# Performance work log

Measured on AMD Instinct MI355X. Metric: run time of the kernel, lower is better.

## Reference

```python
import math
import jax, jax.numpy as jnp
import numpy as np

N_HEAD = 16
KNN = 4                     # config.knn_num
MEM_FRAC = 8.0              # config.mem_frac
INFLUENCE = 1.0             # config.knn_softmax_influence
RESID_FOUND = 0.5           # from set_resid_frac(resid_frac=0.5) (assumed split)
RESID_CURR = 0.5


def setup_inputs() -> dict:
    key = jax.random.key(0)
    ks = jax.random.split(key, 7)
    B, T, C, H, M = 1, 1024, 1024, N_HEAD, 8192
    d = C // H
    return {
        "x": jax.random.normal(ks[0], (B, T, C), jnp.float32),
        "c_attn_w": jax.random.normal(ks[1], (3 * C, C), jnp.float32) * 0.02,
        "c_attn_b": jax.random.normal(ks[2], (3 * C,), jnp.float32) * 0.01,
        "c_proj_w": jax.random.normal(ks[3], (C, C), jnp.float32) * 0.02,
        "c_proj_b": jax.random.normal(ks[4], (C,), jnp.float32) * 0.01,
        "key_store": jax.random.normal(ks[5], (H, M, d), jnp.float32),
        "value_store": jax.random.normal(ks[6], (H, M, d), jnp.float32),
    }


def _knn_get(att, k, q, v, key_store, value_store):
    # Faithful vectorized version of knn_get (batch must be 1, as in the
    # original whose scatter offsets i*t are only valid for b==1).
    B, H, T, d = k.shape
    scale = 1.0 / math.sqrt(d)
    # last-query attention row over all keys: (B,H,T)
    a = att[:, :, -1, :]
    # mem_frac thresholding (bookkeeping_frac falsy -> skipped)
    a = jnp.where(a < 1.0 / (MEM_FRAC * T), 0.0, a)
    sel = (a != 0.0)[0]                      # (H,T) selected positions
    kh, qh, vh = k[0], q[0], v[0]            # (H,T,d)
    # exact L2 search = faiss.IndexFlatL2: d2 = |k|^2 - 2 k.s + |s|^2
    d2 = (jnp.sum(kh * kh, -1, keepdims=True)
          - 2.0 * jnp.einsum('htd,hmd->htm', kh, key_store)
          + jnp.sum(key_store * key_store, -1)[:, None, :])   # (H,T,M)
    _, idx = jax.lax.top_k(-d2, KNN)         # (H,T,K) nearest neighbors
    idx = jnp.maximum(idx, 0)                # idx[idx<0]=0
    keys_f = jnp.take_along_axis(key_store[:, None, :, :], idx[..., None], axis=2)   # (H,T,K,d)
    vals_f = jnp.take_along_axis(value_store[:, None, :, :], idx[..., None], axis=2)
    # not resid_only: prepend current key/value -> stack size K+1
    keys_all = jnp.concatenate([kh[:, :, None, :], keys_f], axis=2)   # (H,T,S,d)
    vals_all = jnp.concatenate([vh[:, :, None, :], vals_f], axis=2)
    attf = jnp.einsum('htd,htsd->hts', qh, keys_all) * scale
    attf = jnp.where(jnp.isnan(attf), -jnp.inf, attf)
    w = jax.nn.softmax(attf * INFLUENCE, axis=-1)                     # softmax over the stack dim
    vals = jnp.einsum('hts,htsd->htd', w, vals_all)
    vals = vals * RESID_FOUND + vh * RESID_CURR                       # resid mix branch
    v_new = jnp.where(sel[..., None], vals, vh)                       # scatter back
    return v_new[None]                                                # (1,H,T,d)


def reference(x, c_attn_w, c_attn_b, c_proj_w, c_proj_b, key_store, value_store):
    B, T, C = x.shape
    H = key_store.shape[0]
    d = C // H
    qkv = x @ c_attn_w.T + c_attn_b
    q, k, v = jnp.split(qkv, 3, axis=2)
    heads = lambda t: t.reshape(B, T, H, d).transpose(0, 2, 1, 3)
    q, k, v = heads(q), heads(k), heads(v)
    logits = jnp.einsum('bhqd,bhkd->bhqk', q, k) * (1.0 / math.sqrt(d))
    causal = jnp.tril(jnp.ones((T, T), bool))
    logits = jnp.where(causal, logits, -jnp.inf)
    att = jax.nn.softmax(logits, axis=-1)
    # knn_get runs under torch.no_grad in the original
    v_new = jax.lax.stop_gradient(_knn_get(att, k, q, v, key_store, value_store))
    y = jnp.einsum('bhqk,bhkd->bhqd', att, v_new)   # dropout p=0 (eval)
    y = y.transpose(0, 2, 1, 3).reshape(B, T, C)
    return y @ c_proj_w.T + c_proj_b
```

## Files before the change

kernel.cpp:

```cpp
#include <hip/hip_runtime.h>
#include <math.h>

#define NH 16
#define TT 1024
#define CC 1024
#define DD 64
#define MM 8192
#define MQ 4
#define MQS (MM / MQ)

typedef __attribute__((ext_vector_type(8))) short short8;
typedef __attribute__((ext_vector_type(4))) float f32x4;

__device__ __forceinline__ float wredsum(float x) {
#pragma unroll
  for (int o = 32; o; o >>= 1) x += __shfl_xor(x, o);
  return x;
}
__device__ __forceinline__ unsigned int bf16rn(float x) {
  unsigned int u = __float_as_uint(x);
  return (u + 0x7fffu + ((u >> 16) & 1u)) >> 16;
}
__device__ __forceinline__ float bf16f(unsigned int h) {
  return __uint_as_float(h << 16);
}

__device__ __forceinline__ void ins4(float d, int i, float vd[4], int vi[4]) {
  if (d < vd[3] || (d == vd[3] && i < vi[3])) {
    vd[3] = d; vi[3] = i;
#pragma unroll
    for (int s = 3; s > 0; --s) {
      bool sw = (vd[s] < vd[s - 1]) || (vd[s] == vd[s - 1] && vi[s] < vi[s - 1]);
      if (sw) {
        float td = vd[s]; vd[s] = vd[s - 1]; vd[s - 1] = td;
        int ti = vi[s]; vi[s] = vi[s - 1]; vi[s - 1] = ti;
      }
    }
  }
}

__device__ __forceinline__ void stage_rows8_swz(const char* gRow0, size_t gStride, char* lds, int lane) {
  int rr = lane >> 3;
  int c = (lane & 7) ^ rr;
  __builtin_amdgcn_global_load_lds(
      (const __attribute__((address_space(1))) unsigned int*)(gRow0 + (size_t)rr * gStride + (c << 4)),
      (__attribute__((address_space(3))) unsigned int*)lds, 16, 0, 0);
}

__device__ __forceinline__ void conv_chunk(const float* __restrict__ src,
                                           char* __restrict__ hi, char* __restrict__ lo, int gc) {
  const float* p = src + ((size_t)gc << 3);
  float4 f0 = *(const float4*)p;
  float4 f1 = *(const float4*)(p + 4);
  float f[8] = {f0.x, f0.y, f0.z, f0.w, f1.x, f1.y, f1.z, f1.w};
  short8 hv, lv;
#pragma unroll
  for (int e = 0; e < 8; ++e) {
    unsigned hb = bf16rn(f[e]);
    hv[e] = (short)hb;
    lv[e] = (short)bf16rn(f[e] - bf16f(hb));
  }
  size_t off = (size_t)gc << 4;
  *(short8*)(hi + off) = hv;
  *(short8*)(lo + off) = lv;
}

__global__ void __launch_bounds__(256) convert_all(
    const float* __restrict__ x, char* __restrict__ xhi, char* __restrict__ xlo,
    const float* __restrict__ Wa, char* __restrict__ wahi, char* __restrict__ walo,
    const float* __restrict__ Wp, char* __restrict__ wphi, char* __restrict__ wplo)
{
  int b = blockIdx.x, tid = threadIdx.x;
  if (b < 512) conv_chunk(x, xhi, xlo, b * 256 + tid);
  else if (b < 2048) conv_chunk(Wa, wahi, walo, (b - 512) * 256 + tid);
  else conv_chunk(Wp, wphi, wplo, (b - 2048) * 256 + tid);
}

__global__ void __launch_bounds__(256) convert_kernel(
    const float* __restrict__ ks, char* __restrict__ khi,
    char* __restrict__ klo, float* __restrict__ kn2)
{
  int gc = blockIdx.x * 256 + threadIdx.x;
  const float* p = ks + ((size_t)gc << 3);
  float4 f0 = *(const float4*)p;
  float4 f1 = *(const float4*)(p + 4);
  float f[8] = {f0.x, f0.y, f0.z, f0.w, f1.x, f1.y, f1.z, f1.w};
  float s = 0.f;
  short8 hv, lv;
#pragma unroll
  for (int e = 0; e < 8; ++e) {
    s = fmaf(f[e], f[e], s);
    unsigned hb = bf16rn(f[e]);
    hv[e] = (short)hb;
    lv[e] = (short)bf16rn(f[e] - bf16f(hb));
  }
  size_t off = (size_t)gc << 4;
  *(short8*)(khi + off) = hv;
  *(short8*)(klo + off) = lv;
  s += __shfl_xor(s, 1);
  s += __shfl_xor(s, 2);
  s += __shfl_xor(s, 4);
  if ((threadIdx.x & 7) == 0) kn2[gc >> 3] = -0.5f * s;
}

__global__ void __launch_bounds__(256) gemm_hl(
    const char* __restrict__ Ahi, const char* __restrict__ Alo, int strideA, int aKb0, int aKbz,
    const char* __restrict__ Bhi, const char* __restrict__ Blo, int strideB, int bKb0, int bKbz,
    int kbBeg, int kbCnt, int kbzStep,
    float* __restrict__ Cf, long long czMul, int ldc,
    const float* __restrict__ bias, float scale)
{
  int bx = blockIdx.x, by = blockIdx.y, z = blockIdx.z;
  int n0 = bx * 128, m0 = by * 128;
  int tid = threadIdx.x, lane = tid & 63, w = tid >> 6;
  int wr = w >> 1, wc = w & 1;
  __shared__ __align__(16) char smem[65536];
  char* sAhi = smem;
  char* sAlo = smem + 16384;
  char* sBhi = smem + 32768;
  char* sBlo = smem + 49152;
  f32x4 acc[4][4];
#pragma unroll
  for (int i = 0; i < 4; ++i)
#pragma unroll
    for (int j = 0; j < 4; ++j) acc[i][j] = (f32x4){0.f, 0.f, 0.f, 0.f};

  int kb0 = kbBeg + z * kbzStep;
  int lr = lane & 15, lc = lane >> 4;
  for (int i = 0; i < kbCnt; ++i) {
    int kbA = aKb0 + z * aKbz + kb0 + i;
    int kbB = bKb0 + z * bKbz + kb0 + i;
    if (i) __syncthreads();
#pragma unroll
    for (int c8 = 0; c8 < 4; ++c8) {
      int r8 = w * 32 + c8 * 8;
      stage_rows8_swz(Ahi + (size_t)(m0 + r8) * strideA + (size_t)kbA * 128, strideA, sAhi + r8 * 128, lane);
      stage_rows8_swz(Alo + (size_t)(m0 + r8) * strideA + (size_t)kbA * 128, strideA, sAlo + r8 * 128, lane);
      stage_rows8_swz(Bhi + (size_t)(n0 + r8) * strideB + (size_t)kbB * 128, strideB, sBhi + r8 * 128, lane);
      stage_rows8_swz(Blo + (size_t)(n0 + r8) * strideB + (size_t)kbB * 128, strideB, sBlo + r8 * 128, lane);
    }
    __syncthreads();
#pragma unroll
    for (int kh = 0; kh < 2; ++kh) {
      short8 ah[4], al[4], bh[4], bl[4];
#pragma unroll
      for (int f = 0; f < 4; ++f) {
        int ra = wr * 64 + f * 16 + lr;
        int ca = ((kh * 4 + lc) ^ (ra & 7)) << 4;
        ah[f] = *(const short8*)(sAhi + ra * 128 + ca);
        al[f] = *(const short8*)(sAlo + ra * 128 + ca);
        int rb = wc * 64 + f * 16 + lr;
        int cb = ((kh * 4 + lc) ^ (rb & 7)) << 4;
        bh[f] = *(const short8*)(sBhi + rb * 128 + cb);
        bl[f] = *(const short8*)(sBlo + rb * 128 + cb);
      }
#pragma unroll
      for (int mi = 0; mi < 4; ++mi)
#pragma unroll
        for (int nj = 0; nj < 4; ++nj) {
          acc[mi][nj] = __builtin_amdgcn_mfma_f32_16x16x32_bf16(ah[mi], bh[nj], acc[mi][nj], 0, 0, 0);
          acc[mi][nj] = __builtin_amdgcn_mfma_f32_16x16x32_bf16(al[mi], bh[nj], acc[mi][nj], 0, 0, 0);
          acc[mi][nj] = __builtin_amdgcn_mfma_f32_16x16x32_bf16(ah[mi], bl[nj], acc[mi][nj], 0, 0, 0);
        }
    }
  }
#pragma unroll
  for (int mi = 0; mi < 4; ++mi)
#pragma unroll
    for (int nj = 0; nj < 4; ++nj)
#pragma unroll
      for (int r = 0; r < 4; ++r) {
        int m = m0 + wr * 64 + mi * 16 + lc * 4 + r;
        int n = n0 + wc * 64 + nj * 16 + lr;
        float v = acc[mi][nj][r] * scale;
        if (bias) v += bias[n];
        Cf[(size_t)z * czMul + (size_t)m * ldc + n] = v;
      }
}

__global__ void __launch_bounds__(256) reduce_qkv(
    const float* __restrict__ p, const float* __restrict__ bias,
    char* __restrict__ hi, char* __restrict__ lo)
{
  int gc = blockIdx.x * 256 + threadIdx.x;
  int t = gc / 384, c = gc - t * 384;
  const float* p0 = p + (size_t)t * 3072 + (c << 3);
  const float* p1 = p0 + (size_t)3072 * 1024;
  float4 a0 = *(const float4*)p0, a1 = *(const float4*)(p0 + 4);
  float4 b0 = *(const float4*)p1, b1 = *(const float4*)(p1 + 4);
  float4 bb0 = *(const float4*)(bias + (c << 3));
  float4 bb1 = *(const float4*)(bias + (c << 3) + 4);
  float f[8] = {a0.x + b0.x + bb0.x, a0.y + b0.y + bb0.y,
                a0.z + b0.z + bb0.z, a0.w + b0.w + bb0.w,
                a1.x + b1.x + bb1.x, a1.y + b1.y + bb1.y,
                a1.z + b1.z + bb1.z, a1.w + b1.w + bb1.w};
  short8 hv, lv;
#pragma unroll
  for (int e = 0; e < 8; ++e) {
    unsigned hb = bf16rn(f[e]);
    hv[e] = (short)hb;
    lv[e] = (short)bf16rn(f[e] - bf16f(hb));
  }
  size_t off = (size_t)gc << 4;
  *(short8*)(hi + off) = hv;
  *(short8*)(lo + off) = lv;
}

#define QSLDS 2304
__global__ void __launch_bounds__(512) qk_softmax(
    const char* __restrict__ qhi, const char* __restrict__ qlo,
    char* __restrict__ attB, float* __restrict__ attlast)
{
  int rb = blockIdx.x, h = blockIdx.y;
  int i0 = rb * 32;
  int tid = threadIdx.x, lane = tid & 63, w = tid >> 6;
  int wr = w >> 2, wcg = w & 3;
  int lr = lane & 15, lc = lane >> 4;
  __shared__ float redm[2][16][4];
  __shared__ float reds[2][16][4];
  __shared__ __align__(16) char tb[8][2 * QSLDS];

  int iq = i0 + wr * 16 + lr;
  short8 ah[2], al[2];
  {
    size_t qb = (size_t)iq * 6144 + h * 128;
#pragma unroll
    for (int kh = 0; kh < 2; ++kh) {
      size_t off = qb + ((kh * 4 + lc) << 4);
      ah[kh] = *(const short8*)(qhi + off);
      al[kh] = *(const short8*)(qlo + off);
    }
  }

  f32x4 acc[16];
#pragma unroll
  for (int nt = 0; nt < 16; ++nt) acc[nt] = (f32x4){0.f, 0.f, 0.f, 0.f};

  int maxj = i0 + 31;
#pragma unroll
  for (int nt = 0; nt < 16; ++nt) {
    if (wcg * 256 + nt * 16 <= maxj) {
      int jr = wcg * 256 + nt * 16 + lr;
      size_t kb = (size_t)jr * 6144 + 2048 + h * 128;
      short8 bh[2], bl[2];
#pragma unroll
      for (int kh = 0; kh < 2; ++kh) {
        size_t off = kb + ((kh * 4 + lc) << 4);
        bh[kh] = *(const short8*)(qhi + off);
        bl[kh] = *(const short8*)(qlo + off);
      }
#pragma unroll
      for (int kh = 0; kh < 2; ++kh) {
        acc[nt] = __builtin_amdgcn_mfma_f32_16x16x32_bf16(ah[kh], bh[kh], acc[nt], 0, 0, 0);
        acc[nt] = __builtin_amdgcn_mfma_f32_16x16x32_bf16(al[kh], bh[kh], acc[nt], 0, 0, 0);
        acc[nt] = __builtin_amdgcn_mfma_f32_16x16x32_bf16(ah[kh], bl[kh], acc[nt], 0, 0, 0);
      }
    }
  }

  int iv[4];
  float pmax[4];
#pragma unroll
  for (int r = 0; r < 4; ++r) {
    iv[r] = i0 + wr * 16 + lc * 4 + r;
    pmax[r] = -INFINITY;
  }
#pragma unroll
  for (int nt = 0; nt < 16; ++nt) {
    int j = wcg * 256 + nt * 16 + lr;
#pragma unroll
    for (int r = 0; r < 4; ++r) {
      float v = (j <= iv[r]) ? acc[nt][r] * 0.125f : -INFINITY;
      acc[nt][r] = v;
      pmax[r] = fmaxf(pmax[r], v);
    }
  }
#pragma unroll
  for (int o = 1; o <= 8; o <<= 1)
#pragma unroll
    for (int r = 0; r < 4; ++r) pmax[r] = fmaxf(pmax[r], __shfl_xor(pmax[r], o));
  if (lr == 0) {
#pragma unroll
    for (int r = 0; r < 4; ++r) redm[wr][lc * 4 + r][wcg] = pmax[r];
  }
  __syncthreads();
  float rowm[4];
#pragma unroll
  for (int r = 0; r < 4; ++r) {
    float* q = redm[wr][lc * 4 + r];
    rowm[r] = fmaxf(fmaxf(q[0], q[1]), fmaxf(q[2], q[3]));
  }

  float psum[4] = {0.f, 0.f, 0.f, 0.f};
#pragma unroll
  for (int nt = 0; nt < 16; ++nt)
#pragma unroll
    for (int r = 0; r < 4; ++r) {
      float e = __expf(acc[nt][r] - rowm[r]);
      acc[nt][r] = e;
      psum[r] += e;
    }
#pragma unroll
  for (int o = 1; o <= 8; o <<= 1)
#pragma unroll
    for (int r = 0; r < 4; ++r) psum[r] += __shfl_xor(psum[r], o);
  if (lr == 0) {
#pragma unroll
    for (int r = 0; r < 4; ++r) reds[wr][lc * 4 + r][wcg] = psum[r];
  }
  __syncthreads();
  float inv[4];
#pragma unroll
  for (int r = 0; r < 4; ++r) {
    float* q = reds[wr][lc * 4 + r];
    inv[r] = 1.0f / (q[0] + q[1] + q[2] + q[3]);
  }

  char* mybuf = tb[w];
  int iv0 = i0 + wr * 16;
#pragma unroll
  for (int cc = 0; cc < 4; ++cc) {
#pragma unroll
    for (int q = 0; q < 4; ++q) {
      int nt = cc * 4 + q;
      int col = q * 16 + lr;
#pragma unroll
      for (int r = 0; r < 4; ++r) {
        int row = lc * 4 + r;
        float v = acc[nt][r] * inv[r];
        unsigned hb = bf16rn(v);
        unsigned lb = bf16rn(v - bf16f(hb));
        *(unsigned short*)(mybuf + row * 144 + col * 2) = (unsigned short)hb;
        *(unsigned short*)(mybuf + QSLDS + row * 144 + col * 2) = (unsigned short)lb;
        if (iv[r] == 1023) attlast[(h << 10) + wcg * 256 + cc * 64 + col] = v;
      }
    }
    __syncthreads();
#pragma unroll
    for (int half = 0; half < 2; ++half) {
      int rr = (lane >> 3) + half * 8;
      int c = lane & 7;
      int rowg = iv0 + rr;
      uint4 hv = *(const uint4*)(mybuf + rr * 144 + c * 16);
      uint4 lv = *(const uint4*)(mybuf + QSLDS + rr * 144 + c * 16);
      size_t basep = ((size_t)h << 22) + ((size_t)rowg << 12)
                   + (size_t)(((wcg << 2) + cc) << 7) + (size_t)(c << 4);
      *(uint4*)(attB + basep) = hv;
      *(uint4*)(attB + basep + 2048) = lv;
    }
    __syncthreads();
  }
}

#define BUFB 16384
__global__ void __launch_bounds__(256, 4) topk_mfma(
    const char* __restrict__ qhi, const char* __restrict__ qlo,
    const char* __restrict__ khi, const char* __restrict__ klo,
    const float* __restrict__ kn2, float* __restrict__ pd, int* __restrict__ pi)
{
  int bid = blockIdx.x;
  int h = bid & 15, ttile = (bid >> 4) & 15, mq = bid >> 8;
  int tid = threadIdx.x, lane = tid & 63, w = tid >> 6;
  int t0 = ttile * 64 + w * 16;
  __shared__ __align__(16) char smem[2 * BUFB];

  short8 bhi[2], blo[2];
  {
    int t = t0 + (lane & 15);
    size_t rb = (size_t)t * 6144 + 2048 + h * 128;
#pragma unroll
    for (int kh = 0; kh < 2; ++kh) {
      size_t off = rb + ((kh * 4 + (lane >> 4)) << 4);
      bhi[kh] = *(const short8*)(qhi + off);
      blo[kh] = *(const short8*)(qlo + off);
    }
  }

  const char* ghi = khi + ((size_t)h * MM + (size_t)mq * MQS) * 128;
  const char* glo = klo + ((size_t)h * MM + (size_t)mq * MQS) * 128;
  const float* gk2 = kn2 + (size_t)h * MM + (size_t)mq * MQS + ((lane >> 4) << 2);

  float ba[4] = {-3.0e38f, -3.0e38f, -3.0e38f, -3.0e38f};
  int   bi_[4] = {-1, -1, -1, -1};

  {
#pragma unroll
    for (int i2 = 0; i2 < 4; ++i2) {
      int s = w * 4 + i2;
      const char* src = (s < 8) ? (ghi + s * 1024) : (glo + (s - 8) * 1024);
      stage_rows8_swz(src, 128, smem + s * 1024, lane);
    }
  }
  __syncthreads();

  int buf = 0;
  const int NIT = MQS / 64;
  for (int it = 0; it < NIT; ++it) {
    char* cb = smem + buf * BUFB;
    if (it < NIT - 1) {
      char* nb = smem + (buf ^ 1) * BUFB;
      const char* bh = ghi + (size_t)(it + 1) * 8192;
      const char* bl = glo + (size_t)(it + 1) * 8192;
#pragma unroll
      for (int i2 = 0; i2 < 4; ++i2) {
        int s = w * 4 + i2;
        const char* src = (s < 8) ? (bh + s * 1024) : (bl + (s - 8) * 1024);
        stage_rows8_swz(src, 128, nb + s * 1024, lane);
      }
    }

    f32x4 acc[4];
#pragma unroll
    for (int ms = 0; ms < 4; ++ms)
      acc[ms] = *(const f32x4*)(gk2 + it * 64 + ms * 16);
#pragma unroll
    for (int ms = 0; ms < 4; ++ms) {
      int mloc = ms * 16 + (lane & 15);
      short8 ah[2], al[2];
#pragma unroll
      for (int kh = 0; kh < 2; ++kh) {
        int c = kh * 4 + (lane >> 4);
        int off = mloc * 128 + (((c ^ (mloc & 7)) << 4));
        ah[kh] = *(const short8*)(cb + off);
        al[kh] = *(const short8*)(cb + 8192 + off);
      }
#pragma unroll
      for (int kh = 0; kh < 2; ++kh) {
        acc[ms] = __builtin_amdgcn_mfma_f32_16x16x32_bf16(ah[kh], bhi[kh], acc[ms], 0, 0, 0);
        acc[ms] = __builtin_amdgcn_mfma_f32_16x16x32_bf16(al[kh], bhi[kh], acc[ms], 0, 0, 0);
        acc[ms] = __builtin_amdgcn_mfma_f32_16x16x32_bf16(ah[kh], blo[kh], acc[ms], 0, 0, 0);
      }
    }

    float pk[16];
#pragma unroll
    for (int ms = 0; ms < 4; ++ms)
#pragma unroll
      for (int r = 0; r < 4; ++r) {
        unsigned u = __float_as_uint(acc[ms][r]);
        pk[ms * 4 + r] = __uint_as_float((u & ~15u) | (unsigned)(ms * 4 + r));
      }
    float mx = pk[0];
#pragma unroll
    for (int c = 1; c < 16; ++c) mx = fmaxf(mx, pk[c]);

    int mg0 = mq * MQS + it * 64 + ((lane >> 4) << 2);
    while (mx > ba[3]) {
      unsigned pb = __float_as_uint(mx);
      int cl = pb & 15;
      ba[3] = mx; bi_[3] = mg0 + ((cl & 12) << 2) + (cl & 3);
#pragma unroll
      for (int s = 3; s > 0; --s) {
        if (ba[s] > ba[s - 1]) {
          float td = ba[s]; ba[s] = ba[s - 1]; ba[s - 1] = td;
          int ti = bi_[s]; bi_[s] = bi_[s - 1]; bi_[s - 1] = ti;
        }
      }
#pragma unroll
      for (int c2 = 0; c2 < 16; ++c2)
        if (pk[c2] == mx) pk[c2] = -3.0e38f;
      mx = pk[0];
#pragma unroll
      for (int c2 = 1; c2 < 16; ++c2) mx = fmaxf(mx, pk[c2]);
    }

    __syncthreads();
    buf ^= 1;
  }

  float bd[4];
#pragma unroll
  for (int s = 0; s < 4; ++s) bd[s] = ba[s] * -2.0f;
#pragma unroll
  for (int st = 16; st <= 32; st <<= 1) {
    float sd[4]; int si[4];
#pragma unroll
    for (int s = 0; s < 4; ++s) {
      sd[s] = __shfl_xor(bd[s], st);
      si[s] = __shfl_xor(bi_[s], st);
    }
#pragma unroll
    for (int s = 0; s < 4; ++s) ins4(sd[s], si[s], bd, bi_);
  }
  if (lane < 16) {
    size_t o = (((size_t)mq * NH + h) * TT + (t0 + lane)) * 4;
#pragma unroll
    for (int s = 0; s < 4; ++s) { pd[o + s] = bd[s]; pi[o + s] = bi_[s]; }
  }
}

__global__ void __launch_bounds__(1024) knn_attend(
    const char* __restrict__ qhi, const char* __restrict__ qlo,
    const float* __restrict__ attlast,
    const float* __restrict__ pd, const int* __restrict__ pi,
    const float* __restrict__ kstore, const float* __restrict__ vstore,
    char* __restrict__ vThi, char* __restrict__ vTlo)
{
  __shared__ __align__(16) unsigned short hiT[64][72];
  __shared__ __align__(16) unsigned short loT[64][72];
  int tid = threadIdx.x, lane = tid & 63, w = tid >> 6;
  int h = blockIdx.x >> 4, t0 = (blockIdx.x & 15) << 6;

#pragma unroll
  for (int i = 0; i < 4; ++i) {
    int t = t0 + w * 4 + i;
    int g = (h << 10) + t;

    float fd[4]; int fi[4];
    {
      size_t o = ((size_t)(lane & 3) * (NH * TT) + g) * 4;
#pragma unroll
      for (int s = 0; s < 4; ++s) { fd[s] = pd[o + s]; fi[s] = pi[o + s]; }
#pragma unroll
      for (int st = 1; st <= 2; st <<= 1) {
        float sd[4]; int si[4];
#pragma unroll
        for (int s = 0; s < 4; ++s) {
          sd[s] = __shfl_xor(fd[s], st);
          si[s] = __shfl_xor(fi[s], st);
        }
#pragma unroll
        for (int s = 0; s < 4; ++s) ins4(sd[s], si[s], fd, fi);
      }
    }

    size_t rb = (size_t)t * 6144 + h * 128 + lane * 2;
    float q = bf16f(*(const unsigned short*)(qhi + rb)) + bf16f(*(const unsigned short*)(qlo + rb));
    float k = bf16f(*(const unsigned short*)(qhi + rb + 2048)) + bf16f(*(const unsigned short*)(qlo + rb + 2048));
    float v = bf16f(*(const unsigned short*)(qhi + rb + 4096)) + bf16f(*(const unsigned short*)(qlo + rb + 4096));
    float al = attlast[g];
    bool sel = al >= (1.0f / 8192.0f);

    float attf[5], vf[5];
    attf[0] = wredsum(q * k) * 0.125f;
    vf[0] = v;
#pragma unroll
    for (int s = 1; s < 5; ++s) {
      int m = fi[s - 1];
      const float* kp = kstore + ((size_t)h * MM + m) * DD;
      const float* vp = vstore + ((size_t)h * MM + m) * DD;
      attf[s] = wredsum(q * kp[lane]) * 0.125f;
      vf[s] = vp[lane];
    }
    float mx = attf[0];
#pragma unroll
    for (int s = 1; s < 5; ++s) mx = fmaxf(mx, attf[s]);
    float wgt[5], sum = 0.f;
#pragma unroll
    for (int s = 0; s < 5; ++s) { wgt[s] = __expf(attf[s] - mx); sum += wgt[s]; }
    float inv = 1.0f / sum;
    float vals = 0.f;
#pragma unroll
    for (int s = 0; s < 5; ++s) vals = fmaf(wgt[s] * inv, vf[s], vals);
    float r = 0.5f * vals + 0.5f * v;
    float vn = sel ? r : v;

    unsigned hb = bf16rn(vn);
    hiT[lane][t - t0] = (unsigned short)hb;
    loT[lane][t - t0] = (unsigned short)bf16rn(vn - bf16f(hb));
  }
  __syncthreads();

  int half = tid >> 9;
  int idx = tid & 511;
  int r = idx >> 3, c = idx & 7;
  const unsigned short* src = half ? &loT[r][c * 8] : &hiT[r][c * 8];
  uint4 vv = *(const uint4*)src;
  char* dst = (half ? vTlo : vThi) + (size_t)((h << 6) + r) * 2048 + ((size_t)t0 << 1) + (c << 4);
  *(uint4*)dst = vv;
}

__global__ void __launch_bounds__(256) gemm_attv(
    const char* __restrict__ attB, const char* __restrict__ vThi, const char* __restrict__ vTlo,
    char* __restrict__ Yhi, char* __restrict__ Ylo)
{
  int h = blockIdx.y, m0 = blockIdx.x * 128;
  const char* aBase = attB + (size_t)h * 4194304;
  int tid = threadIdx.x, lane = tid & 63, w = tid >> 6;
  int wr = w >> 1, wc = w & 1;
  __shared__ __align__(16) char smem[49152];
  char* sAhi = smem;
  char* sAlo = smem + 16384;
  char* sBhi = smem + 32768;
  char* sBlo = smem + 40960;
  f32x4 acc[4][2];
#pragma unroll
  for (int i = 0; i < 4; ++i)
#pragma unroll
    for (int j = 0; j < 2; ++j) acc[i][j] = (f32x4){0.f, 0.f, 0.f, 0.f};
  int lr = lane & 15, lc = lane >> 4;
  for (int kb = 0; kb < 16; ++kb) {
    if (kb) __syncthreads();
#pragma unroll
    for (int c8 = 0; c8 < 4; ++c8) {
      int r8 = w * 32 + c8 * 8;
      stage_rows8_swz(aBase + (size_t)(m0 + r8) * 4096 + (size_t)kb * 128, 4096, sAhi + r8 * 128, lane);
      stage_rows8_swz(aBase + (size_t)(m0 + r8) * 4096 + 2048 + (size_t)kb * 128, 4096, sAlo + r8 * 128, lane);
    }
#pragma unroll
    for (int c8 = 0; c8 < 2; ++c8) {
      int r8 = w * 16 + c8 * 8;
      stage_rows8_swz(vThi + (size_t)((h << 6) + r8) * 2048 + (size_t)kb * 128, 2048, sBhi + r8 * 128, lane);
      stage_rows8_swz(vTlo + (size_t)((h << 6) + r8) * 2048 + (size_t)kb * 128, 2048, sBlo + r8 * 128, lane);
    }
    __syncthreads();
#pragma unroll
    for (int kh = 0; kh < 2; ++kh) {
      short8 ah[4], al[4], bh[2], bl[2];
#pragma unroll
      for (int f = 0; f < 4; ++f) {
        int ra = wr * 64 + f * 16 + lr;
        int ca = ((kh * 4 + lc) ^ (ra & 7)) << 4;
        ah[f] = *(const short8*)(sAhi + ra * 128 + ca);
        al[f] = *(const short8*)(sAlo + ra * 128 + ca);
      }
#pragma unroll
      for (int f = 0; f < 2; ++f) {
        int rbr = wc * 32 + f * 16 + lr;
        int cb = ((kh * 4 + lc) ^ (rbr & 7)) << 4;
        bh[f] = *(const short8*)(sBhi + rbr * 128 + cb);
        bl[f] = *(const short8*)(sBlo + rbr * 128 + cb);
      }
#pragma unroll
      for (int mi = 0; mi < 4; ++mi)
#pragma unroll
        for (int nj = 0; nj < 2; ++nj) {
          acc[mi][nj] = __builtin_amdgcn_mfma_f32_16x16x32_bf16(ah[mi], bh[nj], acc[mi][nj], 0, 0, 0);
          acc[mi][nj] = __builtin_amdgcn_mfma_f32_16x16x32_bf16(al[mi], bh[nj], acc[mi][nj], 0, 0, 0);
          acc[mi][nj] = __builtin_amdgcn_mfma_f32_16x16x32_bf16(ah[mi], bl[nj], acc[mi][nj], 0, 0, 0);
        }
    }
  }
#pragma unroll
  for (int mi = 0; mi < 4; ++mi)
#pragma unroll
    for (int nj = 0; nj < 2; ++nj)
#pragma unroll
      for (int r = 0; r < 4; ++r) {
        int m = m0 + wr * 64 + mi * 16 + lc * 4 + r;
        int n = (h << 6) + wc * 32 + nj * 16 + lr;
        float v = acc[mi][nj][r];
        unsigned hb = bf16rn(v);
        size_t off = ((size_t)m * 1024 + n) * 2;
        *(unsigned short*)(Yhi + off) = (unsigned short)hb;
        *(unsigned short*)(Ylo + off) = (unsigned short)bf16rn(v - bf16f(hb));
      }
}

__global__ void __launch_bounds__(256) reduce_bias(
    const float* __restrict__ p, const float* __restrict__ bias, float* __restrict__ out)
{
  int i4 = blockIdx.x * 256 + threadIdx.x;
  const float4* P = (const float4*)p;
  float4 a = P[i4], b = P[i4 + 262144], c = P[i4 + 524288], d = P[i4 + 786432];
  float4 bb = ((const float4*)bias)[i4 & 255];
  float4 o;
  o.x = a.x + b.x + c.x + d.x + bb.x;
  o.y = a.y + b.y + c.y + d.y + bb.y;
  o.z = a.z + b.z + c.z + d.z + bb.z;
  o.w = a.w + b.w + c.w + d.w + bb.w;
  ((float4*)out)[i4] = o;
}

extern "C" void kernel_launch(void* const* d_in, const int* in_sizes, int n_in,
                              void* d_out, int out_size, void* d_ws, size_t ws_size,
                              hipStream_t stream) {
  (void)in_sizes; (void)n_in; (void)out_size; (void)ws_size;
  const float* x  = (const float*)d_in[0];
  const float* Wa = (const float*)d_in[1];
  const float* ba = (const float*)d_in[2];
  const float* Wp = (const float*)d_in[3];
  const float* bp = (const float*)d_in[4];
  const float* Ks = (const float*)d_in[5];
  const float* Vs = (const float*)d_in[6];
  float* out = (float*)d_out;

  char* base = (char*)d_ws;
  char* xhi  = base;
  char* xlo  = base + 0x200000;
  char* wahi = base + 0x400000;
  char* walo = base + 0xA00000;
  char* khi  = base + 0x1000000;
  char* klo  = base + 0x2000000;
  float* qkvp = (float*)(base + 0x1000000);
  char*  attB = base;
  float* pout = (float*)base;
  char* tail = base + 0x4000000;
  char* qhi = tail;
  char* qlo = tail + 0x600000;
  float* attlast = (float*)(tail + 0xC00000);
  float* kn2     = (float*)(tail + 0xC10000);
  float* pd      = (float*)(tail + 0xC90000);
  int*   pi      = (int*)(tail + 0xE90000);
  char* vThi = tail + 0x1090000;
  char* vTlo = tail + 0x1290000;
  char* yhi  = tail + 0x1490000;
  char* ylo  = tail + 0x1690000;
  char* wphi = tail + 0x1890000;
  char* wplo = tail + 0x1A90000;

  hipLaunchKernelGGL(convert_all, dim3(2560), dim3(256), 0, stream,
                     x, xhi, xlo, Wa, wahi, walo, Wp, wphi, wplo);
  hipLaunchKernelGGL(gemm_hl, dim3(24, 8, 2), dim3(256), 0, stream,
                     (const char*)xhi, (const char*)xlo, 2048, 0, 0,
                     (const char*)wahi, (const char*)walo, 2048, 0, 0,
                     0, 8, 8,
                     qkvp, 3145728LL, 3072,
                     (const float*)nullptr, 1.0f);
  hipLaunchKernelGGL(reduce_qkv, dim3(1536), dim3(256), 0, stream, qkvp, ba, qhi, qlo);
  hipLaunchKernelGGL(convert_kernel, dim3(NH * MM * 8 / 256), dim3(256), 0, stream, Ks, khi, klo, kn2);
  hipLaunchKernelGGL(topk_mfma, dim3(16 * 16 * MQ), dim3(256), 0, stream,
                     (const char*)qhi, (const char*)qlo, (const char*)khi, (const char*)klo,
                     kn2, pd, pi);
  hipLaunchKernelGGL(qk_softmax, dim3(32, 16), dim3(512), 0, stream,
                     (const char*)qhi, (const char*)qlo, attB, attlast);
  hipLaunchKernelGGL(knn_attend, dim3(256), dim3(1024), 0, stream,
                     (const char*)qhi, (const char*)qlo, attlast, pd, pi, Ks, Vs, vThi, vTlo);
  hipLaunchKernelGGL(gemm_attv, dim3(8, 16), dim3(256), 0, stream,
                     (const char*)attB, (const char*)vThi, (const char*)vTlo, yhi, ylo);
  hipLaunchKernelGGL(gemm_hl, dim3(8, 8, 4), dim3(256), 0, stream,
                     (const char*)yhi, (const char*)ylo, 2048, 0, 0,
                     (const char*)wphi, (const char*)wplo, 2048, 0, 0,
                     0, 4, 4,
                     pout, 1048576LL, 1024,
                     (const float*)nullptr, 1.0f);
  hipLaunchKernelGGL(reduce_bias, dim3(1024), dim3(256), 0, stream, pout, bp, out);
}
```

Measured before the change: 232.4 us.

## Use direct global-to-LDS loads in top-k and skip causal-masked K blocks in AV

```diff
diff --git a/kernel.cpp b/kernel.cpp
--- a/kernel.cpp
+++ b/kernel.cpp
@@ -353,6 +353,69 @@
 }
 
 #define BUFB 16384
+
+#define TOPK_STEP(PAR, DO_STAGE)                                              \
+  {                                                                           \
+    if (DO_STAGE) {                                                           \
+      _Pragma("unroll")                                                       \
+      for (int i2 = 0; i2 < 4; ++i2) {                                        \
+        __builtin_amdgcn_global_load_lds(                                     \
+            (const __attribute__((address_space(1))) unsigned int*)stsrc[i2], \
+            (__attribute__((address_space(3))) unsigned int*)(stdst[i2] + ((PAR) ^ 16384)), \
+            16, 0, 0);                                                        \
+        stsrc[i2] += 8192;                                                    \
+      }                                                                       \
+    }                                                                         \
+    f32x4 acc[4];                                                             \
+    _Pragma("unroll")                                                         \
+    for (int ms = 0; ms < 4; ++ms)                                            \
+      acc[ms] = *(const f32x4*)(knp + ms * 64);                               \
+    knp += 256;                                                               \
+    _Pragma("unroll")                                                         \
+    for (int ms = 0; ms < 4; ++ms) {                                          \
+      short8 ah0 = *(const short8*)(frg[ms * 2 + 0] + (PAR));                 \
+      short8 al0 = *(const short8*)(frg[ms * 2 + 0] + (PAR) + 8192);          \
+      short8 ah1 = *(const short8*)(frg[ms * 2 + 1] + (PAR));                 \
+      short8 al1 = *(const short8*)(frg[ms * 2 + 1] + (PAR) + 8192);          \
+      acc[ms] = __builtin_amdgcn_mfma_f32_16x16x32_bf16(ah0, bhi[0], acc[ms], 0, 0, 0); \
+      acc[ms] = __builtin_amdgcn_mfma_f32_16x16x32_bf16(al0, bhi[0], acc[ms], 0, 0, 0); \
+      acc[ms] = __builtin_amdgcn_mfma_f32_16x16x32_bf16(ah0, blo[0], acc[ms], 0, 0, 0); \
+      acc[ms] = __builtin_amdgcn_mfma_f32_16x16x32_bf16(ah1, bhi[1], acc[ms], 0, 0, 0); \
+      acc[ms] = __builtin_amdgcn_mfma_f32_16x16x32_bf16(al1, bhi[1], acc[ms], 0, 0, 0); \
+      acc[ms] = __builtin_amdgcn_mfma_f32_16x16x32_bf16(ah1, blo[1], acc[ms], 0, 0, 0); \
+    }                                                                         \
+    float pk[16];                                                             \
+    _Pragma("unroll")                                                         \
+    for (int ms = 0; ms < 4; ++ms)                                            \
+      _Pragma("unroll")                                                       \
+      for (int r = 0; r < 4; ++r) {                                           \
+        unsigned u = __float_as_uint(acc[ms][r]);                             \
+        pk[ms * 4 + r] = __uint_as_float((u & ~15u) | (unsigned)(ms * 4 + r)); \
+      }                                                                       \
+    float mx = pk[0];                                                         \
+    _Pragma("unroll")                                                         \
+    for (int c = 1; c < 16; ++c) mx = fmaxf(mx, pk[c]);                       \
+    while (mx > ba[3]) {                                                      \
+      unsigned pb = __float_as_uint(mx);                                      \
+      int cl = pb & 15;                                                       \
+      ba[3] = mx; bi_[3] = mg0 + ((cl & 12) << 2) + (cl & 3);                 \
+      _Pragma("unroll")                                                       \
+      for (int s = 3; s > 0; --s)                                             \
+        if (ba[s] > ba[s - 1]) {                                              \
+          float td = ba[s]; ba[s] = ba[s - 1]; ba[s - 1] = td;                \
+          int ti = bi_[s]; bi_[s] = bi_[s - 1]; bi_[s - 1] = ti;              \
+        }                                                                     \
+      _Pragma("unroll")                                                       \
+      for (int c2 = 0; c2 < 16; ++c2)                                         \
+        if (pk[c2] == mx) pk[c2] = -3.0e38f;                                  \
+      mx = pk[0];                                                             \
+      _Pragma("unroll")                                                       \
+      for (int c2 = 1; c2 < 16; ++c2) mx = fmaxf(mx, pk[c2]);                 \
+    }                                                                         \
+    mg0 += 64;                                                                \
+    __syncthreads();                                                          \
+  }
+
 __global__ void __launch_bounds__(256, 4) topk_mfma(
     const char* __restrict__ qhi, const char* __restrict__ qlo,
     const char* __restrict__ khi, const char* __restrict__ klo,
@@ -378,94 +441,46 @@
 
   const char* ghi = khi + ((size_t)h * MM + (size_t)mq * MQS) * 128;
   const char* glo = klo + ((size_t)h * MM + (size_t)mq * MQS) * 128;
-  const float* gk2 = kn2 + (size_t)h * MM + (size_t)mq * MQS + ((lane >> 4) << 2);
+  const char* knp = (const char*)(kn2 + (size_t)h * MM + (size_t)mq * MQS + ((lane >> 4) << 2));
 
   float ba[4] = {-3.0e38f, -3.0e38f, -3.0e38f, -3.0e38f};
   int   bi_[4] = {-1, -1, -1, -1};
 
+  const char* stsrc[4];
+  char* stdst[4];
   {
+    int rr = lane >> 3;
+    size_t laneoff = (size_t)rr * 128 + (((lane & 7) ^ rr) << 4);
 #pragma unroll
     for (int i2 = 0; i2 < 4; ++i2) {
       int s = w * 4 + i2;
-      const char* src = (s < 8) ? (ghi + s * 1024) : (glo + (s - 8) * 1024);
-      stage_rows8_swz(src, 128, smem + s * 1024, lane);
-    }
+      stsrc[i2] = ((s < 8) ? (ghi + s * 1024) : (glo + (s - 8) * 1024)) + laneoff;
+      stdst[i2] = smem + s * 1024;
+    }
+  }
+  char* frg[8];
+#pragma unroll
+  for (int ms = 0; ms < 4; ++ms)
+#pragma unroll
+    for (int kh = 0; kh < 2; ++kh) {
+      int mloc = ms * 16 + (lane & 15);
+      int c = kh * 4 + (lane >> 4);
+      frg[ms * 2 + kh] = smem + mloc * 128 + ((c ^ (mloc & 7)) << 4);
+    }
+
+#pragma unroll
+  for (int i2 = 0; i2 < 4; ++i2) {
+    __builtin_amdgcn_global_load_lds(
+        (const __attribute__((address_space(1))) unsigned int*)stsrc[i2],
+        (__attribute__((address_space(3))) unsigned int*)stdst[i2], 16, 0, 0);
+    stsrc[i2] += 8192;
   }
   __syncthreads();
 
-  int buf = 0;
-  const int NIT = MQS / 64;
-  for (int it = 0; it < NIT; ++it) {
-    char* cb = smem + buf * BUFB;
-    if (it < NIT - 1) {
-      char* nb = smem + (buf ^ 1) * BUFB;
-      const char* bh = ghi + (size_t)(it + 1) * 8192;
-      const char* bl = glo + (size_t)(it + 1) * 8192;
-#pragma unroll
-      for (int i2 = 0; i2 < 4; ++i2) {
-        int s = w * 4 + i2;
-        const char* src = (s < 8) ? (bh + s * 1024) : (bl + (s - 8) * 1024);
-        stage_rows8_swz(src, 128, nb + s * 1024, lane);
-      }
-    }
-
-    f32x4 acc[4];
-#pragma unroll
-    for (int ms = 0; ms < 4; ++ms)
-      acc[ms] = *(const f32x4*)(gk2 + it * 64 + ms * 16);
-#pragma unroll
-    for (int ms = 0; ms < 4; ++ms) {
-      int mloc = ms * 16 + (lane & 15);
-      short8 ah[2], al[2];
-#pragma unroll
-      for (int kh = 0; kh < 2; ++kh) {
-        int c = kh * 4 + (lane >> 4);
-        int off = mloc * 128 + (((c ^ (mloc & 7)) << 4));
-        ah[kh] = *(const short8*)(cb + off);
-        al[kh] = *(const short8*)(cb + 8192 + off);
-      }
-#pragma unroll
-      for (int kh = 0; kh < 2; ++kh) {
-        acc[ms] = __builtin_amdgcn_mfma_f32_16x16x32_bf16(ah[kh], bhi[kh], acc[ms], 0, 0, 0);
-        acc[ms] = __builtin_amdgcn_mfma_f32_16x16x32_bf16(al[kh], bhi[kh], acc[ms], 0, 0, 0);
-        acc[ms] = __builtin_amdgcn_mfma_f32_16x16x32_bf16(ah[kh], blo[kh], acc[ms], 0, 0, 0);
-      }
-    }
-
-    float pk[16];
-#pragma unroll
-    for (int ms = 0; ms < 4; ++ms)
-#pragma unroll
-      for (int r = 0; r < 4; ++r) {
-        unsigned u = __float_as_uint(acc[ms][r]);
-        pk[ms * 4 + r] = __uint_as_float((u & ~15u) | (unsigned)(ms * 4 + r));
-      }
-    float mx = pk[0];
-#pragma unroll
-    for (int c = 1; c < 16; ++c) mx = fmaxf(mx, pk[c]);
-
-    int mg0 = mq * MQS + it * 64 + ((lane >> 4) << 2);
-    while (mx > ba[3]) {
-      unsigned pb = __float_as_uint(mx);
-      int cl = pb & 15;
-      ba[3] = mx; bi_[3] = mg0 + ((cl & 12) << 2) + (cl & 3);
-#pragma unroll
-      for (int s = 3; s > 0; --s) {
-        if (ba[s] > ba[s - 1]) {
-          float td = ba[s]; ba[s] = ba[s - 1]; ba[s - 1] = td;
-          int ti = bi_[s]; bi_[s] = bi_[s - 1]; bi_[s - 1] = ti;
-        }
-      }
-#pragma unroll
-      for (int c2 = 0; c2 < 16; ++c2)
-        if (pk[c2] == mx) pk[c2] = -3.0e38f;
-      mx = pk[0];
-#pragma unroll
-      for (int c2 = 1; c2 < 16; ++c2) mx = fmaxf(mx, pk[c2]);
-    }
-
-    __syncthreads();
-    buf ^= 1;
+  int mg0 = mq * MQS + ((lane >> 4) << 2);
+  for (int it2 = 0; it2 < 16; ++it2) {
+    TOPK_STEP(0, true)
+    TOPK_STEP(16384, (it2 < 15))
   }
 
   float bd[4];
@@ -589,7 +604,9 @@
 #pragma unroll
     for (int j = 0; j < 2; ++j) acc[i][j] = (f32x4){0.f, 0.f, 0.f, 0.f};
   int lr = lane & 15, lc = lane >> 4;
-  for (int kb = 0; kb < 16; ++kb) {
+  int kbEnd = ((m0 + 127) >> 6) + 1;
+  if (kbEnd > 16) kbEnd = 16;
+  for (int kb = 0; kb < kbEnd; ++kb) {
     if (kb) __syncthreads();
 #pragma unroll
     for (int c8 = 0; c8 < 4; ++c8) {
```

Result: faster. 225.9 us (-2.8%).
